# Optimization experiments

Hardware: AMD Instinct MI355X
Metric: run time of the kernel (lower is better)

## Reference

```python
import jax, jax.numpy as jnp
import numpy as np

N = 4096      # (num_domains+1) * batch_size
F_IN = 512    # nfeat
HID = 64      # nhid per head
H = 8         # nheads
ALPHA = 0.2   # leaky-relu negative slope
EDGE_P = 0.01 # adjacency density


def setup_inputs() -> dict:
    key = jax.random.key(0)
    k1, k2, k3, k4 = jax.random.split(key, 4)
    x = jax.random.normal(k1, (N, F_IN), dtype=jnp.float32)
    adj = (jax.random.uniform(k2, (N, N)) < EDGE_P).astype(jnp.float32)
    # ensure self-loops so every row has at least one valid edge for softmax
    adj = jnp.maximum(adj, jnp.eye(N, dtype=jnp.float32))
    W = jax.random.normal(k3, (H, F_IN, HID), dtype=jnp.float32) * 0.1
    a = jax.random.normal(k4, (H, 2 * HID), dtype=jnp.float32) * 0.1
    return {"x": x, "adj": adj, "W": W, "a": a}


def reference(x, adj, W, a):
    # Wh: [H, N, HID] -- per-head linear projection
    Wh = jnp.einsum('nf,hfd->hnd', x, W)
    # additive attention logits: e_ij = leakyrelu(a1.Wh_i + a2.Wh_j)
    e_src = jnp.einsum('hnd,hd->hn', Wh, a[:, :HID])   # [H, N]
    e_dst = jnp.einsum('hnd,hd->hn', Wh, a[:, HID:])   # [H, N]
    e = jax.nn.leaky_relu(e_src[:, :, None] + e_dst[:, None, :], ALPHA)  # [H, N, N]
    e = jnp.where(adj[None] > 0, e, jnp.float32(-9e15))
    att = jax.nn.softmax(e, axis=-1)                    # masked softmax over neighbors
    h = jnp.einsum('hnm,hmd->hnd', att, Wh)             # [H, N, HID]
    h = jax.nn.elu(h)                                   # concat=True -> elu per head
    # concat heads: [N, H*HID]
    return jnp.transpose(h, (1, 0, 2)).reshape(N, H * HID)
```

## Files before the change

kernel.cpp:

```cpp
#include <hip/hip_runtime.h>
#include <hip/hip_bf16.h>
#include <math.h>

#define N_NODES 4096
#define F_IN    512
#define HID     64
#define H       8
#define NJ      512
#define ALPHA   0.2f

typedef __bf16 bf16x8 __attribute__((ext_vector_type(8)));
typedef float  f32x4  __attribute__((ext_vector_type(4)));

#define A_UNITS (N_NODES * F_IN / 4)
#define B_UNITS (NJ * F_IN)

__device__ __forceinline__ void split_bf16(float v, __bf16& hi, __bf16& lo) {
    hi = (__bf16)v;
    lo = (__bf16)(v - (float)hi);
}

__global__ __launch_bounds__(256) void conv_prep(const float* __restrict__ x,
                                                 const float* __restrict__ W,
                                                 __bf16* __restrict__ Ah,
                                                 __bf16* __restrict__ Al,
                                                 __bf16* __restrict__ Bth,
                                                 __bf16* __restrict__ Btl) {
    int id = blockIdx.x * 256 + threadIdx.x;
    if (id < A_UNITS) {
        float4 v = ((const float4*)x)[id];
        __bf16 h0, h1, h2, h3, l0, l1, l2, l3;
        split_bf16(v.x, h0, l0); split_bf16(v.y, h1, l1);
        split_bf16(v.z, h2, l2); split_bf16(v.w, h3, l3);
        __bf16* ph = Ah + (size_t)id * 4;
        __bf16* pl = Al + (size_t)id * 4;
        ph[0] = h0; ph[1] = h1; ph[2] = h2; ph[3] = h3;
        pl[0] = l0; pl[1] = l1; pl[2] = l2; pl[3] = l3;
    } else {
        int bid = id - A_UNITS;
        if (bid < B_UNITS) {
            int k = bid & (F_IN - 1);
            int j = bid >> 9;
            float v = W[(size_t)(j >> 6) * F_IN * HID + (size_t)k * HID + (j & 63)];
            __bf16 h, l;
            split_bf16(v, h, l);
            Bth[(size_t)j * F_IN + k] = h;
            Btl[(size_t)j * F_IN + k] = l;
        }
    }
}

__global__ __launch_bounds__(256) void wh_gemm_fused(const __bf16* __restrict__ Ah,
                                                     const __bf16* __restrict__ Al,
                                                     const __bf16* __restrict__ Bth,
                                                     const float* __restrict__ a,
                                                     __bf16* __restrict__ Whb,
                                                     float* __restrict__ esrc,
                                                     float* __restrict__ edst) {
    const int bm = blockIdx.x;
    const int h  = blockIdx.y;
    const int tid  = threadIdx.x;
    const int wave = tid >> 6;
    const int lane = tid & 63;
    const int lm = lane & 15;
    const int lq = lane >> 4;

    __shared__ __align__(16) __bf16 As_h[64][72];
    __shared__ __align__(16) __bf16 As_l[64][72];
    __shared__ __align__(16) __bf16 Bs_h[64][72];

    f32x4 acc[4];
    #pragma unroll
    for (int c = 0; c < 4; c++) acc[c] = (f32x4){0.f, 0.f, 0.f, 0.f};

    for (int k0 = 0; k0 < F_IN; k0 += 64) {
        #pragma unroll
        for (int s = 0; s < 2; s++) {
            int idx = tid + s * 256;
            int m  = idx >> 3;
            int kk = (idx & 7) << 3;
            size_t ga = (size_t)(bm * 64 + m) * F_IN + k0 + kk;
            size_t gb = (size_t)(h * 64 + m) * F_IN + k0 + kk;
            *(uint4*)&As_h[m][kk] = *(const uint4*)(Ah + ga);
            *(uint4*)&As_l[m][kk] = *(const uint4*)(Al + ga);
            *(uint4*)&Bs_h[m][kk] = *(const uint4*)(Bth + gb);
        }
        __syncthreads();

        #pragma unroll
        for (int kh = 0; kh < 2; kh++) {
            bf16x8 afh = *(const bf16x8*)&As_h[wave * 16 + lm][kh * 32 + lq * 8];
            bf16x8 afl = *(const bf16x8*)&As_l[wave * 16 + lm][kh * 32 + lq * 8];
            bf16x8 bh[4];
            #pragma unroll
            for (int c = 0; c < 4; c++) {
                bh[c] = *(const bf16x8*)&Bs_h[c * 16 + lm][kh * 32 + lq * 8];
            }
            #pragma unroll
            for (int c = 0; c < 4; c++) {
                acc[c] = __builtin_amdgcn_mfma_f32_16x16x32_bf16(afh, bh[c], acc[c], 0, 0, 0);
                acc[c] = __builtin_amdgcn_mfma_f32_16x16x32_bf16(afl, bh[c], acc[c], 0, 0, 0);
            }
        }
        __syncthreads();
    }

    float a1c[4], a2c[4];
    #pragma unroll
    for (int c = 0; c < 4; c++) {
        a1c[c] = a[h * 2 * HID + c * 16 + lm];
        a2c[c] = a[h * 2 * HID + HID + c * 16 + lm];
    }

    #pragma unroll
    for (int r = 0; r < 4; r++) {
        int row = bm * 64 + wave * 16 + lq * 4 + r;
        float s1 = 0.f, s2 = 0.f;
        #pragma unroll
        for (int c = 0; c < 4; c++) {
            float v = acc[c][r];
            Whb[(size_t)row * NJ + h * HID + c * 16 + lm] = (__bf16)v;
            s1 += v * a1c[c];
            s2 += v * a2c[c];
        }
        #pragma unroll
        for (int o = 1; o < 16; o <<= 1) {
            s1 += __shfl_xor(s1, o);
            s2 += __shfl_xor(s2, o);
        }
        if (lm == 0) {
            esrc[h * N_NODES + row] = s1;
            edst[h * N_NODES + row] = s2;
        }
    }
}

#define MAXN 128

__global__ __launch_bounds__(512) void gat_attn(const float* __restrict__ adj,
                                                const __bf16* __restrict__ Whb,
                                                const float* __restrict__ esrc,
                                                const float* __restrict__ edst,
                                                float* __restrict__ out) {
    const int i    = blockIdx.x;
    const int tid  = threadIdx.x;
    const int wave = tid >> 6;
    const int lane = tid & 63;
    __shared__ int    nbr[MAXN];
    __shared__ __align__(8)  float2 an[H][MAXN];
    __shared__ float  denom[H];
    __shared__ __align__(16) float4 part[3][128];
    __shared__ int    cnt;

    if (tid == 0) cnt = 0;
    __syncthreads();

    const unsigned long long lt = (1ull << lane) - 1ull;
    const float4* arow = (const float4*)(adj + (size_t)i * N_NODES);
    #pragma unroll
    for (int cc = 0; cc < 2; cc++) {
        int chunk = wave * 2 + cc;
        float4 q = arow[chunk * 64 + lane];
        unsigned long long b0 = __ballot(q.x > 0.f);
        unsigned long long b1 = __ballot(q.y > 0.f);
        unsigned long long b2 = __ballot(q.z > 0.f);
        unsigned long long b3 = __ballot(q.w > 0.f);
        int c0 = __popcll(b0), c1 = __popcll(b1), c2 = __popcll(b2), c3 = __popcll(b3);
        int base = 0;
        if (lane == 0) base = atomicAdd(&cnt, c0 + c1 + c2 + c3);
        base = __shfl(base, 0);
        int col = chunk * 256 + lane * 4;
        if (q.x > 0.f) nbr[base + __popcll(b0 & lt)] = col;
        base += c0;
        if (q.y > 0.f) nbr[base + __popcll(b1 & lt)] = col + 1;
        base += c1;
        if (q.z > 0.f) nbr[base + __popcll(b2 & lt)] = col + 2;
        base += c2;
        if (q.w > 0.f) nbr[base + __popcll(b3 & lt)] = col + 3;
    }
    __syncthreads();
    const int n = cnt;

    {
        float es = esrc[wave * N_NODES + i];
        float m = -1e30f;
        for (int j = lane; j < n; j += 64) {
            int c = nbr[j];
            float lg = es + edst[wave * N_NODES + c];
            lg = lg > 0.f ? lg : ALPHA * lg;
            an[wave][j] = make_float2(lg, __int_as_float(c << 10));
            m = fmaxf(m, lg);
        }
        #pragma unroll
        for (int o = 32; o; o >>= 1) m = fmaxf(m, __shfl_xor(m, o));
        float s = 0.f;
        for (int j = lane; j < n; j += 64) {
            float w = __expf(an[wave][j].x - m);
            an[wave][j].x = w;
            s += w;
        }
        #pragma unroll
        for (int o = 32; o; o >>= 1) s += __shfl_xor(s, o);
        if (lane == 0) denom[wave] = s;
    }
    __syncthreads();

    const int qd = tid >> 7;
    const int t  = tid & 127;
    const int h  = t >> 4;
    const char* wp = (const char*)Whb + t * 8;
    float a0 = 0.f, a1 = 0.f, a2 = 0.f, a3 = 0.f;
    #pragma unroll 2
    for (int j = qd; j < n; j += 4) {
        float2 p = an[h][j];
        uint2 u = *(const uint2*)(wp + __float_as_uint(p.y));
        float w = p.x;
        a0 += w * __uint_as_float(u.x << 16);
        a1 += w * __uint_as_float(u.x & 0xffff0000u);
        a2 += w * __uint_as_float(u.y << 16);
        a3 += w * __uint_as_float(u.y & 0xffff0000u);
    }
    if (qd) part[qd - 1][t] = make_float4(a0, a1, a2, a3);
    __syncthreads();
    if (qd == 0) {
        #pragma unroll
        for (int q = 0; q < 3; q++) {
            float4 p = part[q][t];
            a0 += p.x; a1 += p.y; a2 += p.z; a3 += p.w;
        }
        float inv = 1.f / denom[h];
        a0 *= inv; a1 *= inv; a2 *= inv; a3 *= inv;
        a0 = a0 > 0.f ? a0 : expm1f(a0);
        a1 = a1 > 0.f ? a1 : expm1f(a1);
        a2 = a2 > 0.f ? a2 : expm1f(a2);
        a3 = a3 > 0.f ? a3 : expm1f(a3);
        *(float4*)(out + (size_t)i * NJ + t * 4) = make_float4(a0, a1, a2, a3);
    }
}

extern "C" void kernel_launch(void* const* d_in, const int* in_sizes, int n_in,
                              void* d_out, int out_size, void* d_ws, size_t ws_size,
                              hipStream_t stream) {
    const float* x   = (const float*)d_in[0];
    const float* adj = (const float*)d_in[1];
    const float* W   = (const float*)d_in[2];
    const float* a   = (const float*)d_in[3];
    float* out = (float*)d_out;

    float*  esrc = (float*)d_ws;
    float*  edst = esrc + (size_t)H * N_NODES;
    __bf16* Whb  = (__bf16*)(edst + (size_t)H * N_NODES);
    __bf16* Ah   = Whb + (size_t)N_NODES * NJ;
    __bf16* Al   = Ah  + (size_t)N_NODES * F_IN;
    __bf16* Bth  = Al  + (size_t)N_NODES * F_IN;
    __bf16* Btl  = Bth + (size_t)NJ * F_IN;

    conv_prep<<<(A_UNITS + B_UNITS) / 256, 256, 0, stream>>>(x, W, Ah, Al, Bth, Btl);

    dim3 g1(N_NODES / 64, H);
    wh_gemm_fused<<<g1, 256, 0, stream>>>(Ah, Al, Bth, a, Whb, esrc, edst);

    gat_attn<<<N_NODES, 512, 0, stream>>>(adj, Whb, esrc, edst, out);
}
```

Baseline: 137.3 us.

## Split adjacency scan into separate wide kernel and drop unused Btl write

Moves the adjacency-row neighbor compaction out of the per-row attention kernel into a standalone grid-wide kernel that writes neighbor lists and counts to global memory, so the 64MB adjacency read runs at full device parallelism instead of being serialized at the head of each attention block. The attention kernel now only loads a compacted list. It also stops writing the unused low-part of the transposed W. The extra launch and global neighbor buffer add overhead, and the neighbor order within a row becomes nondeterministic across waves.

```diff
diff --git a/kernel.cpp b/kernel.cpp
--- a/kernel.cpp
+++ b/kernel.cpp
@@ -8,6 +8,7 @@
 #define H       8
 #define NJ      512
 #define ALPHA   0.2f
+#define MAXN    128
 
 typedef __bf16 bf16x8 __attribute__((ext_vector_type(8)));
 typedef float  f32x4  __attribute__((ext_vector_type(4)));
@@ -25,8 +26,9 @@
                                                  __bf16* __restrict__ Ah,
                                                  __bf16* __restrict__ Al,
                                                  __bf16* __restrict__ Bth,
-                                                 __bf16* __restrict__ Btl) {
+                                                 int* __restrict__ cnt) {
     int id = blockIdx.x * 256 + threadIdx.x;
+    if (id < N_NODES) cnt[id] = 0;
     if (id < A_UNITS) {
         float4 v = ((const float4*)x)[id];
         __bf16 h0, h1, h2, h3, l0, l1, l2, l3;
@@ -45,7 +47,6 @@
             __bf16 h, l;
             split_bf16(v, h, l);
             Bth[(size_t)j * F_IN + k] = h;
-            Btl[(size_t)j * F_IN + k] = l;
         }
     }
 }
@@ -135,9 +136,43 @@
     }
 }
 
-#define MAXN 128
-
-__global__ __launch_bounds__(512) void gat_attn(const float* __restrict__ adj,
+__global__ __launch_bounds__(256) void scan_adj(const float* __restrict__ adj,
+                                                int* __restrict__ cnt,
+                                                int* __restrict__ nbrg) {
+    const int gw   = (blockIdx.x * 256 + threadIdx.x) >> 6;
+    const int lane = threadIdx.x & 63;
+    const int row  = gw >> 4;
+    const unsigned long long lt = (1ull << lane) - 1ull;
+
+    float4 q = ((const float4*)adj)[(size_t)gw * 64 + lane];
+    unsigned long long b0 = __ballot(q.x > 0.f);
+    unsigned long long b1 = __ballot(q.y > 0.f);
+    unsigned long long b2 = __ballot(q.z > 0.f);
+    unsigned long long b3 = __ballot(q.w > 0.f);
+    int c0 = __popcll(b0), c1 = __popcll(b1), c2 = __popcll(b2), c3 = __popcll(b3);
+    int tot = c0 + c1 + c2 + c3;
+    if (tot == 0) return;
+    int base = 0;
+    if (lane == 0) base = atomicAdd(&cnt[row], tot);
+    base = __shfl(base, 0);
+    int* dst = nbrg + (size_t)row * MAXN;
+    int col = ((gw & 15) * 64 + lane) * 4;
+    int p;
+    p = base + __popcll(b0 & lt);
+    if (q.x > 0.f && p < MAXN) dst[p] = col;
+    base += c0;
+    p = base + __popcll(b1 & lt);
+    if (q.y > 0.f && p < MAXN) dst[p] = col + 1;
+    base += c1;
+    p = base + __popcll(b2 & lt);
+    if (q.z > 0.f && p < MAXN) dst[p] = col + 2;
+    base += c2;
+    p = base + __popcll(b3 & lt);
+    if (q.w > 0.f && p < MAXN) dst[p] = col + 3;
+}
+
+__global__ __launch_bounds__(512) void gat_attn(const int* __restrict__ cnt,
+                                                const int* __restrict__ nbrg,
                                                 const __bf16* __restrict__ Whb,
                                                 const float* __restrict__ esrc,
                                                 const float* __restrict__ edst,
@@ -150,36 +185,11 @@
     __shared__ __align__(8)  float2 an[H][MAXN];
     __shared__ float  denom[H];
     __shared__ __align__(16) float4 part[3][128];
-    __shared__ int    cnt;
-
-    if (tid == 0) cnt = 0;
+
+    int n = cnt[i];
+    if (n > MAXN) n = MAXN;
+    if (tid < n) nbr[tid] = nbrg[(size_t)i * MAXN + tid];
     __syncthreads();
-
-    const unsigned long long lt = (1ull << lane) - 1ull;
-    const float4* arow = (const float4*)(adj + (size_t)i * N_NODES);
-    #pragma unroll
-    for (int cc = 0; cc < 2; cc++) {
-        int chunk = wave * 2 + cc;
-        float4 q = arow[chunk * 64 + lane];
-        unsigned long long b0 = __ballot(q.x > 0.f);
-        unsigned long long b1 = __ballot(q.y > 0.f);
-        unsigned long long b2 = __ballot(q.z > 0.f);
-        unsigned long long b3 = __ballot(q.w > 0.f);
-        int c0 = __popcll(b0), c1 = __popcll(b1), c2 = __popcll(b2), c3 = __popcll(b3);
-        int base = 0;
-        if (lane == 0) base = atomicAdd(&cnt, c0 + c1 + c2 + c3);
-        base = __shfl(base, 0);
-        int col = chunk * 256 + lane * 4;
-        if (q.x > 0.f) nbr[base + __popcll(b0 & lt)] = col;
-        base += c0;
-        if (q.y > 0.f) nbr[base + __popcll(b1 & lt)] = col + 1;
-        base += c1;
-        if (q.z > 0.f) nbr[base + __popcll(b2 & lt)] = col + 2;
-        base += c2;
-        if (q.w > 0.f) nbr[base + __popcll(b3 & lt)] = col + 3;
-    }
-    __syncthreads();
-    const int n = cnt;
 
     {
         float es = esrc[wave * N_NODES + i];
@@ -253,12 +263,15 @@
     __bf16* Ah   = Whb + (size_t)N_NODES * NJ;
     __bf16* Al   = Ah  + (size_t)N_NODES * F_IN;
     __bf16* Bth  = Al  + (size_t)N_NODES * F_IN;
-    __bf16* Btl  = Bth + (size_t)NJ * F_IN;
-
-    conv_prep<<<(A_UNITS + B_UNITS) / 256, 256, 0, stream>>>(x, W, Ah, Al, Bth, Btl);
+    int*    cnt  = (int*)(Bth + (size_t)NJ * F_IN);
+    int*    nbrg = cnt + N_NODES;
+
+    conv_prep<<<(A_UNITS + B_UNITS) / 256, 256, 0, stream>>>(x, W, Ah, Al, Bth, cnt);
 
     dim3 g1(N_NODES / 64, H);
     wh_gemm_fused<<<g1, 256, 0, stream>>>(Ah, Al, Bth, a, Whb, esrc, edst);
 
-    gat_attn<<<N_NODES, 512, 0, stream>>>(adj, Whb, esrc, edst, out);
-}
+    scan_adj<<<(N_NODES * 16) / 4, 256, 0, stream>>>(adj, cnt, nbrg);
+
+    gat_attn<<<N_NODES, 512, 0, stream>>>(cnt, nbrg, Whb, esrc, edst, out);
+}
```

Result: slower. 159.5 us (+16.2%).
